# Performance work log

Hardware: AMD Instinct MI355X
Metric: run time of the kernel (lower is better)

Reference implementation:

```python
import jax, jax.numpy as jnp
import numpy as np

THRESHOLDS = (0.3, 0.4, 0.5)
EPS_NORM = 1e-12   # F.normalize eps
EPS_MAX = 1e-5     # added to max before rescale


def setup_inputs() -> dict:
    key = jax.random.key(0)
    k1, k2 = jax.random.split(key)
    cam = jax.random.uniform(k1, (4, 64, 64), dtype=jnp.float32)
    feat = jax.random.normal(k2, (4, 256, 64, 64), dtype=jnp.float32)
    return {"cam": cam, "feat": feat}


def reference(cam, feat):
    # multi-threshold soft mask: mean of hard masks at each threshold -> (B,1,H,W)
    masks = jnp.stack([(cam >= t).astype(feat.dtype) for t in THRESHOLDS], axis=1)
    m = masks.mean(axis=1)[:, None]  # (B,1,H,W)
    masked = feat * m  # (B,C,H,W)

    B, C, H, W = masked.shape
    f = masked.reshape(B, C, H * W)  # (B,C,N)
    # L2-normalize over channel dim (torch F.normalize, dim=1)
    norm = jnp.sqrt(jnp.sum(f * f, axis=1, keepdims=True))
    fn = f / jnp.maximum(norm, EPS_NORM)

    # full pairwise similarity (B,N,N), then CAM-weighted aggregation
    sim = jnp.einsum('bcn,bcm->bnm', fn, fn)      # (B,N,N)
    camf = cam.reshape(B, H * W)                  # (B,N)
    out = jnp.einsum('bnm,bm->bn', sim, camf)     # (B,N)

    mn = out.min(axis=1, keepdims=True)
    mx = out.max(axis=1, keepdims=True) + EPS_MAX
    ref = ((out - mn) / (mx - mn)).reshape(B, H, W)

    loss = jnp.mean(jnp.abs(ref - jax.lax.stop_gradient(cam)))
    return ref, loss
```

## Files before the change

### kernel.cpp

```cpp
#include <hip/hip_runtime.h>


constexpr int B    = 4;
constexpr int C    = 256;
constexpr int N    = 4096;
constexpr int BN   = B * N;
constexpr int CN   = C * N;
constexpr int NBLK = 512;

#define SCOPE_AGENT __HIP_MEMORY_SCOPE_AGENT

__device__ __forceinline__ float wsum(float v) {
#pragma unroll
    for (int o = 32; o > 0; o >>= 1) v += __shfl_down(v, o, 64);
    return v;
}
__device__ __forceinline__ float wmin64(float v) {
#pragma unroll
    for (int o = 32; o > 0; o >>= 1) v = fminf(v, __shfl_down(v, o, 64));
    return v;
}
__device__ __forceinline__ float wmax64(float v) {
#pragma unroll
    for (int o = 32; o > 0; o >>= 1) v = fmaxf(v, __shfl_down(v, o, 64));
    return v;
}

__global__ void __launch_bounds__(256) k_norm_vpart(
    const float* __restrict__ cam, const float* __restrict__ feat,
    float* __restrict__ s, float* __restrict__ v_part,
    unsigned int* __restrict__ cnt)
{
    if (blockIdx.x == 0 && threadIdx.x == 0) *cnt = 0u;

    __shared__ float tile[C * 33];
    __shared__ float red[8][33];
    __shared__ float w_sh[32];

    const int t   = threadIdx.x;
    const int pix = t & 31;
    const int g   = t >> 5;
    const int bk  = blockIdx.x;
    const int b   = bk >> 7;
    const int n0  = (bk * 32) & (N - 1);

    {
        const float* fp = feat + (size_t)b * CN + (size_t)(g * 32) * N + n0 + pix;
        float ss = 0.f;
#pragma unroll
        for (int cc = 0; cc < 32; ++cc) {
            float x = fp[(size_t)cc * N];
            ss = fmaf(x, x, ss);
            tile[(g * 32 + cc) * 33 + pix] = x;
        }
        red[g][pix] = ss;
    }
    __syncthreads();
    if (t < 32) {
        float tot = 0.f;
#pragma unroll
        for (int gg = 0; gg < 8; ++gg) tot += red[gg][t];
        float cv = cam[bk * 32 + t];
        float m  = ((cv >= 0.3f ? 1.f : 0.f) + (cv >= 0.4f ? 1.f : 0.f) +
                    (cv >= 0.5f ? 1.f : 0.f)) * (1.f / 3.f);
        float sc = m / fmaxf(m * sqrtf(tot), 1e-12f);
        s[bk * 32 + t] = sc;
        w_sh[t] = sc * cv;
    }
    __syncthreads();
    {
        float acc = 0.f;
#pragma unroll
        for (int pp = 0; pp < 32; ++pp)
            acc = fmaf(tile[t * 33 + pp], w_sh[pp], acc);
        v_part[bk * 256 + t] = acc;
    }
}

__global__ void __launch_bounds__(256) k_vreduce(
    const float* __restrict__ v_part, float* __restrict__ v)
{
    __shared__ float vred[4][64];
    const int t  = threadIdx.x;
    const int l  = t & 63;
    const int ks = t >> 6;
    const int bc = blockIdx.x * 64 + l;
    const int vb = bc >> 8, c = bc & 255;
    const float* vp = v_part + (size_t)vb * (128 * 256) + c;
    float a = 0.f;
#pragma unroll
    for (int kk = 0; kk < 32; ++kk)
        a += vp[(size_t)(ks * 32 + kk) * 256];
    vred[ks][l] = a;
    __syncthreads();
    if (t < 64)
        v[bc] = (vred[0][t] + vred[1][t]) + (vred[2][t] + vred[3][t]);
}

__global__ void __launch_bounds__(256) k_out(
    const float* __restrict__ feat, const float* __restrict__ s,
    const float* __restrict__ v, float* __restrict__ ob,
    float* __restrict__ bmn, float* __restrict__ bmx)
{
    const int t   = threadIdx.x;
    const int pix = t & 31;
    const int g   = t >> 5;
    const int bk  = blockIdx.x;
    const int b   = bk >> 7;
    const int n0  = (bk * 32) & (N - 1);

    __shared__ float vs[C];
    vs[t] = v[b * C + t];
    __syncthreads();

    const float* fp = feat + (size_t)b * CN + (size_t)(g * 32) * N + n0 + pix;
    float acc = 0.f;
#pragma unroll 8
    for (int cc = 0; cc < 32; ++cc)
        acc = fmaf(fp[(size_t)cc * N], vs[g * 32 + cc], acc);

    __shared__ float red[8][33];
    red[g][pix] = acc;
    __syncthreads();
    if (t < 32) {
        float tot = 0.f;
#pragma unroll
        for (int gg = 0; gg < 8; ++gg) tot += red[gg][t];
        float o = s[bk * 32 + t] * tot;
        ob[bk * 32 + t] = o;
        float mn = o, mx = o;
#pragma unroll
        for (int o2 = 16; o2 > 0; o2 >>= 1) {
            mn = fminf(mn, __shfl_down(mn, o2, 64));
            mx = fmaxf(mx, __shfl_down(mx, o2, 64));
        }
        if (t == 0) { bmn[bk] = mn; bmx[bk] = mx; }
    }
}

__global__ void __launch_bounds__(256) k_final(
    const float* __restrict__ ob, const float* __restrict__ cam,
    const float* __restrict__ bmn, const float* __restrict__ bmx,
    float* __restrict__ out, float* __restrict__ part, unsigned int* __restrict__ cnt)
{
    const int t = threadIdx.x, blk = blockIdx.x;
    const int p = blk * 256 + t;
    const int b = blk >> 4;

    __shared__ float sh[2];
    if (t < 64) {
        float a = fminf(bmn[b * 128 + t], bmn[b * 128 + 64 + t]);
        a = wmin64(a);
        if (t == 0) sh[0] = a;
    } else if (t < 128) {
        int l = t - 64;
        float a = fmaxf(bmx[b * 128 + l], bmx[b * 128 + 64 + l]);
        a = wmax64(a);
        if (l == 0) sh[1] = a;
    }
    __syncthreads();
    const float mn = sh[0];
    const float mx = sh[1] + 1e-5f;

    float r = (ob[p] - mn) / (mx - mn);
    out[p] = r;
    float ad = fabsf(r - cam[p]);

    __shared__ float red[4];
    float ps = wsum(ad);
    if ((t & 63) == 0) red[t >> 6] = ps;
    __syncthreads();

    __shared__ int lastflag;
    if (t == 0) {
        float tot = (red[0] + red[1]) + (red[2] + red[3]);
        __hip_atomic_store(&part[blk], tot, __ATOMIC_RELEASE, SCOPE_AGENT);
        unsigned old = __hip_atomic_fetch_add(cnt, 1u, __ATOMIC_ACQ_REL, SCOPE_AGENT);
        lastflag = (old == 63u) ? 1 : 0;
    }
    __syncthreads();
    if (lastflag && t < 64) {
        float x = __hip_atomic_load(&part[t], __ATOMIC_ACQUIRE, SCOPE_AGENT);
        x = wsum(x);
        if (t == 0) out[BN] = x * (1.f / (float)BN);
    }
}

extern "C" void kernel_launch(void* const* d_in, const int* in_sizes, int n_in,
                              void* d_out, int out_size, void* d_ws, size_t ws_size,
                              hipStream_t stream) {
    const float* cam  = (const float*)d_in[0];
    const float* feat = (const float*)d_in[1];
    float* out = (float*)d_out;
    float* ws  = (float*)d_ws;

    float* s      = ws;
    float* v_part = ws + 16384;
    float* v      = ws + 147456;
    float* ob     = ws + 148480;
    float* bmn    = ws + 164864;
    float* bmx    = ws + 165376;
    float* part   = ws + 165888;
    unsigned int* cnt = (unsigned int*)(ws + 165952);

    k_norm_vpart<<<NBLK, 256, 0, stream>>>(cam, feat, s, v_part, cnt);
    k_vreduce   <<<16,   256, 0, stream>>>(v_part, v);
    k_out       <<<NBLK, 256, 0, stream>>>(feat, s, v, ob, bmn, bmx);
    k_final     <<<64,   256, 0, stream>>>(ob, cam, bmn, bmx, out, part, cnt);
}
```

Measured before the change: 18.90 us.

## Vectorize feature loads as float4 and keep tile in registers

Both feature-reading kernels now have each thread load float4 chunks covering 4 pixels across 8 channels, in place of scalar loads of one pixel across 32 channels. In the first kernel the loaded values stay in registers, which removes the large shared-memory tile, and the per-channel weighted sums are reduced with 8-lane shuffles. The intent is fewer, wider global memory transactions and less LDS pressure, allowing more blocks per CU. The cost is more registers per thread and a longer 32-way shared reduction for the per-pixel totals.

Result: no change. 19.00 us (+0.6%).

```diff
diff --git a/kernel.cpp b/kernel.cpp
--- a/kernel.cpp
+++ b/kernel.cpp
@@ -33,33 +33,37 @@
 {
     if (blockIdx.x == 0 && threadIdx.x == 0) *cnt = 0u;
 
-    __shared__ float tile[C * 33];
-    __shared__ float red[8][33];
+    __shared__ float red4[32][33];
     __shared__ float w_sh[32];
 
-    const int t   = threadIdx.x;
-    const int pix = t & 31;
-    const int g   = t >> 5;
-    const int bk  = blockIdx.x;
-    const int b   = bk >> 7;
-    const int n0  = (bk * 32) & (N - 1);
-
-    {
-        const float* fp = feat + (size_t)b * CN + (size_t)(g * 32) * N + n0 + pix;
-        float ss = 0.f;
-#pragma unroll
-        for (int cc = 0; cc < 32; ++cc) {
-            float x = fp[(size_t)cc * N];
-            ss = fmaf(x, x, ss);
-            tile[(g * 32 + cc) * 33 + pix] = x;
-        }
-        red[g][pix] = ss;
-    }
-    __syncthreads();
+    const int t  = threadIdx.x;
+    const int qu = t & 7;
+    const int G  = t >> 3;
+    const int bk = blockIdx.x;
+    const int b  = bk >> 7;
+    const int n0 = (bk * 32) & (N - 1);
+
+    const float* fp = feat + (size_t)b * CN + n0 + qu * 4;
+    float4 x[8];
+    float4 ss = make_float4(0.f, 0.f, 0.f, 0.f);
+#pragma unroll
+    for (int it = 0; it < 8; ++it) {
+        x[it] = *(const float4*)(fp + (size_t)(it * 32 + G) * N);
+        ss.x = fmaf(x[it].x, x[it].x, ss.x);
+        ss.y = fmaf(x[it].y, x[it].y, ss.y);
+        ss.z = fmaf(x[it].z, x[it].z, ss.z);
+        ss.w = fmaf(x[it].w, x[it].w, ss.w);
+    }
+    red4[G][qu * 4 + 0] = ss.x;
+    red4[G][qu * 4 + 1] = ss.y;
+    red4[G][qu * 4 + 2] = ss.z;
+    red4[G][qu * 4 + 3] = ss.w;
+    __syncthreads();
+
     if (t < 32) {
         float tot = 0.f;
 #pragma unroll
-        for (int gg = 0; gg < 8; ++gg) tot += red[gg][t];
+        for (int g = 0; g < 32; ++g) tot += red4[g][t];
         float cv = cam[bk * 32 + t];
         float m  = ((cv >= 0.3f ? 1.f : 0.f) + (cv >= 0.4f ? 1.f : 0.f) +
                     (cv >= 0.5f ? 1.f : 0.f)) * (1.f / 3.f);
@@ -68,12 +72,22 @@
         w_sh[t] = sc * cv;
     }
     __syncthreads();
-    {
-        float acc = 0.f;
-#pragma unroll
-        for (int pp = 0; pp < 32; ++pp)
-            acc = fmaf(tile[t * 33 + pp], w_sh[pp], acc);
-        v_part[bk * 256 + t] = acc;
+
+    float4 wq = *(const float4*)&w_sh[qu * 4];
+    float vp[8];
+#pragma unroll
+    for (int it = 0; it < 8; ++it) {
+        float a = fmaf(x[it].x, wq.x,
+                  fmaf(x[it].y, wq.y,
+                  fmaf(x[it].z, wq.z, x[it].w * wq.w)));
+#pragma unroll
+        for (int o = 4; o > 0; o >>= 1) a += __shfl_down(a, o, 8);
+        vp[it] = a;
+    }
+    if (qu == 0) {
+#pragma unroll
+        for (int it = 0; it < 8; ++it)
+            v_part[bk * 256 + it * 32 + G] = vp[it];
     }
 }
 
@@ -102,30 +116,40 @@
     const float* __restrict__ v, float* __restrict__ ob,
     float* __restrict__ bmn, float* __restrict__ bmx)
 {
-    const int t   = threadIdx.x;
-    const int pix = t & 31;
-    const int g   = t >> 5;
-    const int bk  = blockIdx.x;
-    const int b   = bk >> 7;
-    const int n0  = (bk * 32) & (N - 1);
-
     __shared__ float vs[C];
+    __shared__ float red4[32][33];
+
+    const int t  = threadIdx.x;
+    const int qu = t & 7;
+    const int G  = t >> 3;
+    const int bk = blockIdx.x;
+    const int b  = bk >> 7;
+    const int n0 = (bk * 32) & (N - 1);
+
     vs[t] = v[b * C + t];
     __syncthreads();
 
-    const float* fp = feat + (size_t)b * CN + (size_t)(g * 32) * N + n0 + pix;
-    float acc = 0.f;
-#pragma unroll 8
-    for (int cc = 0; cc < 32; ++cc)
-        acc = fmaf(fp[(size_t)cc * N], vs[g * 32 + cc], acc);
-
-    __shared__ float red[8][33];
-    red[g][pix] = acc;
-    __syncthreads();
+    const float* fp = feat + (size_t)b * CN + n0 + qu * 4;
+    float4 acc = make_float4(0.f, 0.f, 0.f, 0.f);
+#pragma unroll
+    for (int it = 0; it < 8; ++it) {
+        float4 xx = *(const float4*)(fp + (size_t)(it * 32 + G) * N);
+        float vc = vs[it * 32 + G];
+        acc.x = fmaf(xx.x, vc, acc.x);
+        acc.y = fmaf(xx.y, vc, acc.y);
+        acc.z = fmaf(xx.z, vc, acc.z);
+        acc.w = fmaf(xx.w, vc, acc.w);
+    }
+    red4[G][qu * 4 + 0] = acc.x;
+    red4[G][qu * 4 + 1] = acc.y;
+    red4[G][qu * 4 + 2] = acc.z;
+    red4[G][qu * 4 + 3] = acc.w;
+    __syncthreads();
+
     if (t < 32) {
         float tot = 0.f;
 #pragma unroll
-        for (int gg = 0; gg < 8; ++gg) tot += red[gg][t];
+        for (int g = 0; g < 32; ++g) tot += red4[g][t];
         float o = s[bk * 32 + t] * tot;
         ob[bk * 32 + t] = o;
         float mn = o, mx = o;
```
